# Performance work log

Hardware: AMD Instinct MI355X
Metric: run time of the kernel (lower is better)

Reference implementation:

```python
import jax, jax.numpy as jnp
import numpy as np

S_D, I_D, O_D = 512, 256, 256
BATCH, T = 64, 1024
SNR = 10.0  # noise scale divisor, as in sample_stable_system
SPECTRAL_RADIUS = 0.95  # stable F, mirroring sample_stable_state_matrix


def setup_inputs() -> dict:
    key = jax.random.key(0)
    ks = jax.random.split(key, 9)
    A = np.asarray(jax.random.normal(ks[0], (S_D, S_D), dtype=jnp.float32))
    F = jnp.asarray(A * (SPECTRAL_RADIUS / np.linalg.norm(A, 2)))  # scale to spectral norm 0.95
    B_mat = jax.random.normal(ks[1], (S_D, I_D), dtype=jnp.float32)
    H = jax.random.normal(ks[2], (O_D, S_D), dtype=jnp.float32)
    sqrt_S_W = jax.random.normal(ks[3], (S_D, S_D), dtype=jnp.float32) / SNR
    sqrt_S_V = jax.random.normal(ks[4], (O_D, O_D), dtype=jnp.float32) / SNR
    state = jax.random.normal(ks[5], (BATCH, S_D), dtype=jnp.float32)
    inputs = jax.random.normal(ks[6], (BATCH, T, I_D), dtype=jnp.float32)
    W_noise = jax.random.normal(ks[7], (BATCH, T, S_D), dtype=jnp.float32)
    V_noise = jax.random.normal(ks[8], (BATCH, T, O_D), dtype=jnp.float32)
    return {"state": state, "inputs": inputs, "W_noise": W_noise, "V_noise": V_noise,
            "F": F, "B_mat": B_mat, "H": H, "sqrt_S_W": sqrt_S_W, "sqrt_S_V": sqrt_S_V}


def reference(state, inputs, W_noise, V_noise, F, B_mat, H, sqrt_S_W, sqrt_S_V):
    # Process noise W = eps_W @ sqrt_S_W.T, measurement noise V = eps_V @ sqrt_S_V.T
    W = jnp.einsum('bti,ji->btj', W_noise, sqrt_S_W)          # (B, T, S_D)
    V = jnp.einsum('bti,ji->btj', V_noise, sqrt_S_V)          # (B, T, O_D)
    drive = jnp.einsum('bti,ji->btj', inputs, B_mat) + W      # u_t @ B.T + W_t

    def step(s, u):  # s_t = s_{t-1} @ F.T + u_t
        s = s @ F.T + u
        return s, s

    _, states_t = jax.lax.scan(step, state, jnp.swapaxes(drive, 0, 1))  # (T, B, S_D)
    states = jnp.swapaxes(states_t, 0, 1)                                # (B, T, S_D)
    observations = jnp.einsum('bts,os->bto', states, H) + V              # (B, T, O_D)
    return states, observations
```

## Files before the change

kernel.cpp:

```cpp
#include <hip/hip_runtime.h>
#include <hip/hip_bf16.h>


typedef short bfrag __attribute__((ext_vector_type(8)));
typedef float f32x4 __attribute__((ext_vector_type(4)));

__device__ __host__ inline unsigned short f2bf(float f) {
    union { float f; unsigned u; } x; x.f = f;
    unsigned r = x.u + 0x7fffu + ((x.u >> 16) & 1u);
    return (unsigned short)(r >> 16);
}
__device__ inline float bf2f(unsigned short h) {
    union { unsigned u; float f; } x; x.u = ((unsigned)h) << 16;
    return x.f;
}

#define MSL 262144L

struct GemmDesc {
    const unsigned short* a0; const unsigned short* a1;
    const unsigned short* b;
    float* c;
    const unsigned short* cmbeta;
    unsigned short* cm;
    unsigned short* cmT;
    long a0_base, a0_os, a0_is;
    long a1_base, a1_os, a1_is;
    long a_zq, a_zr;
    long b_base, b_ldb, b_zq, b_zr;
    long c_base, c_os, c_is, c_zq, c_zr;
    long cm_base, cmb_base, cmT_base;
    long a_shift;
    int a0_icl, a1_icl, c_icl, zdivl;
    int ksplit, K, beta;
    int gxl, gyl, gz_main;
    const unsigned short* xa; const unsigned short* xb;
    unsigned short* xcm; unsigned short* xcmT;
};

template<int BM, int BN>
__global__ __launch_bounds__(256) void gemm_k(GemmDesc d) {
    constexpr int MT = BM / 32;
    constexpr int NT = BN / 32;
    __shared__ __align__(16) unsigned short As[2][BM * 64];
    __shared__ __align__(16) unsigned short Bs[2][BN * 64];
    const int tid  = threadIdx.x;
    const int lane = tid & 63;
    const int w    = tid >> 6;
    const int wrow = (w >> 1) * (BM / 2), wcol = (w & 1) * (BN / 2);

    const unsigned nx = gridDim.x, ny = gridDim.y;
    const unsigned nwg = nx * ny * gridDim.z;
    unsigned wid = blockIdx.x + nx * (blockIdx.y + ny * blockIdx.z);
    if ((nwg & 7) == 0) wid = (wid & 7) * (nwg >> 3) + (wid >> 3);
    const int bx = wid & (nx - 1);
    const int by = (wid >> d.gxl) & (ny - 1);
    int bz = wid >> (d.gxl + d.gyl);

    if (bz >= d.gz_main) {
        if (by >= (512 / BM)) return;
        const long za = (long)(bz - d.gz_main) * MSL;
        d.a0 = d.xa; d.a0_base = za; d.a0_os = 512; d.a0_is = 0; d.a0_icl = 0;
        d.a1 = nullptr;
        d.b = d.xb; d.b_base = 0; d.b_ldb = 512; d.b_zq = d.b_zr = 0;
        d.K = 512; d.ksplit = 1 << 30; d.beta = 0; d.a_shift = 0;
        d.a_zq = d.a_zr = 0;
        d.c = nullptr; d.cm = d.xcm; d.cm_base = za;
        d.c_os = 512; d.c_is = 0; d.c_icl = 0; d.c_zq = d.c_zr = 0; d.c_base = 0;
        d.cmT = d.xcmT; d.cmT_base = za;
        bz = 0;
    }
    const long zq = (long)bz >> d.zdivl;
    const long zr = (long)bz & ((1L << d.zdivl) - 1);
    const int row0 = by * BM;
    const int col0 = bx * BN;

    const int g_r = tid >> 3;
    const int g_k = (tid & 7) * 8;
    const int swz = (g_r & 7) << 3;
    const long za_ = zq * d.a_zq + zr * d.a_zr;
    const long zb_ = zq * d.b_zq + zr * d.b_zr;

    const long m0a = (1L << d.a0_icl) - 1, m1a = (1L << d.a1_icl) - 1;
    long a0off[MT], a1off[MT], boff[NT];
#pragma unroll
    for (int i = 0; i < MT; ++i) {
        long ar = (long)row0 + i * 32 + g_r - d.a_shift;
        if (ar < 0) ar = 0;
        a0off[i] = d.a0_base + za_ + (ar >> d.a0_icl) * d.a0_os + (ar & m0a) * d.a0_is;
        a1off[i] = d.a1 ? (d.a1_base + za_ + (ar >> d.a1_icl) * d.a1_os + (ar & m1a) * d.a1_is) : 0;
    }
#pragma unroll
    for (int i = 0; i < NT; ++i)
        boff[i] = d.b_base + zb_ + (long)(col0 + i * 32 + g_r) * d.b_ldb;

    bfrag ar_[MT], br_[NT];
    auto LOADT = [&](int t) {
        const int k0 = t * 64;
        const bool s1 = (k0 >= d.ksplit);
        const int kb = (s1 ? k0 - d.ksplit : k0) + g_k;
        const unsigned short* sp = s1 ? d.a1 : d.a0;
#pragma unroll
        for (int i = 0; i < MT; ++i)
            ar_[i] = *(const bfrag*)(sp + (s1 ? a1off[i] : a0off[i]) + kb);
#pragma unroll
        for (int i = 0; i < NT; ++i) br_[i] = *(const bfrag*)(d.b + boff[i] + k0 + g_k);
    };
    auto WRT = [&](int buf) {
#pragma unroll
        for (int i = 0; i < MT; ++i)
            *(bfrag*)&As[buf][(i * 32 + g_r) * 64 + (g_k ^ swz)] = ar_[i];
#pragma unroll
        for (int i = 0; i < NT; ++i)
            *(bfrag*)&Bs[buf][(i * 32 + g_r) * 64 + (g_k ^ swz)] = br_[i];
    };

    f32x4 acc[MT][NT] = {};
    const int nt = d.K / 64;

    LOADT(0); WRT(0); __syncthreads();
    int cur = 0;
    for (int t = 0; t < nt; ++t) {
        if (t + 1 < nt) LOADT(t + 1);
#pragma unroll
        for (int ks = 0; ks < 2; ++ks) {
            const int kk = ks * 32 + (lane >> 4) * 8;
            bfrag af[MT], bf_[NT];
#pragma unroll
            for (int mt = 0; mt < MT; ++mt) {
                const int r = wrow + mt * 16 + (lane & 15);
                af[mt] = *(const bfrag*)&As[cur][r * 64 + (kk ^ ((r & 7) << 3))];
            }
#pragma unroll
            for (int nn = 0; nn < NT; ++nn) {
                const int r = wcol + nn * 16 + (lane & 15);
                bf_[nn] = *(const bfrag*)&Bs[cur][r * 64 + (kk ^ ((r & 7) << 3))];
            }
#pragma unroll
            for (int mt = 0; mt < MT; ++mt)
#pragma unroll
                for (int nn = 0; nn < NT; ++nn)
                    acc[mt][nn] = __builtin_amdgcn_mfma_f32_16x16x32_bf16(
                        af[mt], bf_[nn], acc[mt][nn], 0, 0, 0);
        }
        if (t + 1 < nt) WRT(cur ^ 1);
        __syncthreads();
        cur ^= 1;
    }

    const long zc = zq * d.c_zq + zr * d.c_zr;
    const long mc = (1L << d.c_icl) - 1;
#pragma unroll
    for (int mt = 0; mt < MT; ++mt) {
        const int rb = row0 + wrow + mt * 16 + ((lane >> 4) << 2);
#pragma unroll
        for (int nn = 0; nn < NT; ++nn) {
            const int cc = col0 + wcol + nn * 16 + (lane & 15);
#pragma unroll
            for (int j = 0; j < 4; ++j) {
                const long r = rb + j;
                const long off = zc + (r >> d.c_icl) * d.c_os + (r & mc) * d.c_is + cc;
                float v = (r < d.a_shift) ? 0.0f : acc[mt][nn][j];
                if (d.beta == 2) v += bf2f(d.cmbeta[d.cmb_base + off]);
                if (d.c)  d.c[d.c_base + off] = v;
                if (d.cm) d.cm[d.cm_base + off] = f2bf(v);
                if (d.cmT) d.cmT[d.cmT_base + zc + (long)cc * 512 + r] = f2bf(v);
            }
        }
    }
}

__global__ __launch_bounds__(512) void p3obs_k(
        const unsigned short* __restrict__ carry, const unsigned short* __restrict__ Gm,
        const unsigned short* __restrict__ Smir, const unsigned short* __restrict__ BopO,
        const float* __restrict__ Vn, float* __restrict__ states, float* __restrict__ obs) {
    __shared__ __align__(16) unsigned char lds[163840];
    unsigned short* As1 = (unsigned short*)(lds);
    unsigned short* Bs1 = (unsigned short*)(lds + 16384);
    unsigned short* Sb  = (unsigned short*)(lds);
    unsigned short* A2  = (unsigned short*)(lds);
    unsigned short* Ts  = (unsigned short*)(lds + 131072);

    const int tid  = threadIdx.x;
    const int lane = tid & 63;
    const int w    = tid >> 6;
    const int wm   = w >> 2, wn = w & 3;
    const int by   = blockIdx.y;
    const int k    = blockIdx.z;
    const unsigned short* G = Gm + (long)k * MSL;

    f32x4 acc[4][8] = {};

    for (int kt = 0; kt < 8; ++kt) {
        __syncthreads();
#pragma unroll
        for (int i = 0; i < 2; ++i) {
            const int fi = tid + i * 512;
            const int row = fi >> 3, kk = (fi & 7) * 8;
            const long rg = (long)by * 128 + row;
            const long c = rg >> 6, b = rg & 63;
            bfrag v = *(const bfrag*)(carry + c * 32768 + b * 512 + kt * 64 + kk);
            *(bfrag*)&As1[row * 64 + (kk ^ ((row & 7) << 3))] = v;
        }
#pragma unroll
        for (int i = 0; i < 8; ++i) {
            const int fi = tid + i * 512;
            const int row = fi >> 3, kk = (fi & 7) * 8;
            bfrag v = *(const bfrag*)(G + (long)row * 512 + kt * 64 + kk);
            *(bfrag*)&Bs1[row * 64 + (kk ^ ((row & 7) << 3))] = v;
        }
        __syncthreads();
#pragma unroll
        for (int ks = 0; ks < 2; ++ks) {
            const int kk = ks * 32 + (lane >> 4) * 8;
            bfrag af[4], bf_[8];
#pragma unroll
            for (int mt = 0; mt < 4; ++mt) {
                const int r = wm * 64 + mt * 16 + (lane & 15);
                af[mt] = *(const bfrag*)&As1[r * 64 + (kk ^ ((r & 7) << 3))];
            }
#pragma unroll
            for (int nt = 0; nt < 8; ++nt) {
                const int n = wn * 128 + nt * 16 + (lane & 15);
                bf_[nt] = *(const bfrag*)&Bs1[n * 64 + (kk ^ ((n & 7) << 3))];
            }
#pragma unroll
            for (int mt = 0; mt < 4; ++mt)
#pragma unroll
                for (int nt = 0; nt < 8; ++nt)
                    acc[mt][nt] = __builtin_amdgcn_mfma_f32_16x16x32_bf16(
                        af[mt], bf_[nt], acc[mt][nt], 0, 0, 0);
        }
    }
    __syncthreads();

#pragma unroll
    for (int mt = 0; mt < 4; ++mt) {
#pragma unroll
        for (int nt = 0; nt < 8; ++nt) {
#pragma unroll
            for (int j = 0; j < 4; ++j) {
                const int lr = wm * 64 + mt * 16 + ((lane >> 4) << 2) + j;
                const int cc = wn * 128 + nt * 16 + (lane & 15);
                const long rg = (long)by * 128 + lr;
                const long c = rg >> 6, b = rg & 63;
                const long t = c * 8 + k;
                float v = acc[mt][nt][j] + bf2f(Smir[b * 524288L + t * 512 + cc]);
                states[b * 524288L + t * 512 + cc] = v;
                Sb[lr * 512 + (cc ^ ((lr & 7) << 3))] = f2bf(v);
            }
        }
    }

    f32x4 acc2[4][4] = {};
    for (int kt = 0; kt < 12; ++kt) {
        __syncthreads();
#pragma unroll
        for (int i = 0; i < 4; ++i) {
            const int fi = tid + i * 512;
            const int row = fi >> 3, kk = (fi & 7) * 8;
            bfrag v = *(const bfrag*)(BopO + (long)row * 768 + kt * 64 + kk);
            *(bfrag*)&Ts[row * 64 + (kk ^ ((row & 7) << 3))] = v;
        }
        if (kt >= 8) {
#pragma unroll
            for (int i = 0; i < 2; ++i) {
                const int fi = tid + i * 512;
                const int row = fi >> 3, kk = (fi & 7) * 8;
                const long rg = (long)by * 128 + row;
                const long c = rg >> 6, b = rg & 63;
                const long t = c * 8 + k;
                const float* p = Vn + b * 262144L + t * 256 + (kt - 8) * 64 + kk;
                f32x4 x0 = *(const f32x4*)p, x1 = *(const f32x4*)(p + 4);
                union { bfrag v; unsigned short h[8]; } u;
#pragma unroll
                for (int q = 0; q < 4; ++q) { u.h[q] = f2bf(x0[q]); u.h[4 + q] = f2bf(x1[q]); }
                *(bfrag*)&A2[row * 64 + (kk ^ ((row & 7) << 3))] = u.v;
            }
        }
        __syncthreads();
#pragma unroll
        for (int ks = 0; ks < 2; ++ks) {
            const int kk = ks * 32 + (lane >> 4) * 8;
            bfrag af[4], bf_[4];
#pragma unroll
            for (int mt = 0; mt < 4; ++mt) {
                const int r = wm * 64 + mt * 16 + (lane & 15);
                af[mt] = (kt < 8)
                    ? *(const bfrag*)&Sb[r * 512 + ((kt * 64 + kk) ^ ((r & 7) << 3))]
                    : *(const bfrag*)&A2[r * 64 + (kk ^ ((r & 7) << 3))];
            }
#pragma unroll
            for (int nt = 0; nt < 4; ++nt) {
                const int n = wn * 64 + nt * 16 + (lane & 15);
                bf_[nt] = *(const bfrag*)&Ts[n * 64 + (kk ^ ((n & 7) << 3))];
            }
#pragma unroll
            for (int mt = 0; mt < 4; ++mt)
#pragma unroll
                for (int nt = 0; nt < 4; ++nt)
                    acc2[mt][nt] = __builtin_amdgcn_mfma_f32_16x16x32_bf16(
                        af[mt], bf_[nt], acc2[mt][nt], 0, 0, 0);
        }
    }
#pragma unroll
    for (int mt = 0; mt < 4; ++mt) {
#pragma unroll
        for (int nt = 0; nt < 4; ++nt) {
#pragma unroll
            for (int j = 0; j < 4; ++j) {
                const int lr = wm * 64 + mt * 16 + ((lane >> 4) << 2) + j;
                const int cc = wn * 64 + nt * 16 + (lane & 15);
                const long rg = (long)by * 128 + lr;
                const long c = rg >> 6, b = rg & 63;
                const long t = c * 8 + k;
                obs[b * 262144L + t * 256 + cc] = acc2[mt][nt][j];
            }
        }
    }
}

__global__ void cvt_k(const float* src, unsigned short* dst, long n) {
    long i = ((long)blockIdx.x * 256 + threadIdx.x) * 8;
    const long stride = (long)gridDim.x * 256 * 8;
    for (; i < n; i += stride) {
        f32x4 x0 = *(const f32x4*)(src + i), x1 = *(const f32x4*)(src + i + 4);
        union { bfrag v; unsigned short h[8]; } t;
#pragma unroll
        for (int q = 0; q < 4; ++q) { t.h[q] = f2bf(x0[q]); t.h[4 + q] = f2bf(x1[q]); }
        *(bfrag*)(dst + i) = t.v;
    }
}

__global__ void build_ops_k(const float* F, const float* Bm, const float* H,
                            const float* sW, const float* sV,
                            unsigned short* bopd, unsigned short* bopo,
                            unsigned short* G1, unsigned short* Gt1) {
    int i = blockIdx.x * 256 + threadIdx.x;
    const int n1 = 512 * 768, n2 = 256 * 768, n3 = 512 * 512;
    if (i < n1) { int n = i / 768, k = i % 768;
        bopd[i] = f2bf(k < 256 ? Bm[n * 256 + k] : sW[n * 512 + (k - 256)]); return; }
    i -= n1;
    if (i < n2) { int o = i / 768, k = i % 768;
        bopo[i] = f2bf(k < 512 ? H[o * 512 + k] : sV[o * 256 + (k - 512)]); return; }
    i -= n2;
    if (i < n3) { G1[i] = f2bf(F[i]); return; }
    i -= n3;
    if (i < n3) { int r = i / 512, c = i % 512; Gt1[i] = f2bf(F[c * 512 + r]); }
}

__global__ void init_carry_k(const float* st0, const unsigned short* Smir,
                             unsigned short* dst) {
    const long i8 = ((long)blockIdx.x * 256 + threadIdx.x) * 8;
    if (i8 >= 4194304L) return;
    const long c = i8 >> 15, rem = i8 & 32767L;
    const long b = rem >> 9, s = rem & 511L;
    union { bfrag v; unsigned short h[8]; } t;
    if (c == 0) {
        const float* p = st0 + b * 512 + s;
        f32x4 x0 = *(const f32x4*)p, x1 = *(const f32x4*)(p + 4);
#pragma unroll
        for (int q = 0; q < 4; ++q) { t.h[q] = f2bf(x0[q]); t.h[4 + q] = f2bf(x1[q]); }
    } else {
        t.v = *(const bfrag*)(Smir + b * 524288L + (c - 1) * 4096L + 3584L + s);
    }
    *(bfrag*)(dst + i8) = t.v;
}

static GemmDesc D0() {
    GemmDesc d = {};
    d.zdivl = 30;
    d.ksplit = 1 << 30;
    d.b_ldb = 512; d.K = 512;
    d.gz_main = 1 << 30;
    return d;
}

extern "C" void kernel_launch(void* const* d_in, const int* in_sizes, int n_in,
                              void* d_out, int out_size, void* d_ws, size_t ws_size,
                              hipStream_t stream) {
    const float* st0 = (const float*)d_in[0];
    const float* inp = (const float*)d_in[1];
    const float* Wn  = (const float*)d_in[2];
    const float* Vn  = (const float*)d_in[3];
    const float* F   = (const float*)d_in[4];
    const float* Bm  = (const float*)d_in[5];
    const float* H   = (const float*)d_in[6];
    const float* sW  = (const float*)d_in[7];
    const float* sV  = (const float*)d_in[8];

    float* states = (float*)d_out;
    float* obs    = states + 33554432L;

    const long MS = MSL;
    const long CB = 32768;
    const int  NC = 128;
    const int  CL = 8;
    const long TOS = 524288;
    const long COS = (long)CL * 512;

    unsigned short* inpb = (unsigned short*)states;
    unsigned short* Wnb  = inpb + 16777216L;

    unsigned short* Smir = (unsigned short*)d_ws;
    unsigned short* G    = Smir + 33554432L;
    unsigned short* Gt   = G + 8 * MS;
    unsigned short* Qb   = Gt + 8 * MS;
    unsigned short* Qtb  = Qb + 6 * MS;
    unsigned short* BopD = Qtb + 6 * MS;
    unsigned short* BopO = BopD + 512 * 768;
    unsigned short* a0m  = BopO + 256 * 768;
    unsigned short* a1m  = a0m + (long)NC * CB;
    (void)in_sizes; (void)n_in; (void)out_size; (void)ws_size;

    auto L128 = [&](const GemmDesc& d, int gx, int gxl, int gy, int gyl, int gz) {
        GemmDesc dd = d; dd.gxl = gxl; dd.gyl = gyl;
        gemm_k<128, 128><<<dim3(gx, gy, gz), dim3(256), 0, stream>>>(dd);
    };
    auto L64 = [&](const GemmDesc& d, int gx, int gxl, int gy, int gyl, int gz) {
        GemmDesc dd = d; dd.gxl = gxl; dd.gyl = gyl;
        gemm_k<64, 64><<<dim3(gx, gy, gz), dim3(256), 0, stream>>>(dd);
    };

    cvt_k<<<dim3(2048), dim3(256), 0, stream>>>(inp, inpb, 16777216L);
    cvt_k<<<dim3(2048), dim3(256), 0, stream>>>(Wn, Wnb, 33554432L);

    build_ops_k<<<dim3(4352), dim3(256), 0, stream>>>(F, Bm, H, sW, sV, BopD, BopO, G, Gt);

    {
        GemmDesc d = D0();
        d.a0 = inpb; d.a0_os = 256;
        d.a1 = Wnb;  d.a1_os = 512;
        d.ksplit = 256; d.K = 768;
        d.b = BopD; d.b_ldb = 768;
        d.cm = Smir; d.c_os = 512;
        L128(d, 4, 2, 512, 9, 1);
    }

    for (int k = 1; k < CL; ++k) {
        GemmDesc d = D0();
        d.a0 = Smir; d.a0_base = (long)(k - 1) * 512;
        d.a0_icl = 7; d.a0_is = COS; d.a0_os = TOS;
        d.b = G;
        d.c_base = (long)k * 512;
        d.c_icl = 7; d.c_is = COS; d.c_os = TOS;
        d.beta = 2; d.cmbeta = Smir; d.cmb_base = (long)k * 512;
        d.cm = Smir; d.cm_base = (long)k * 512;
        d.gz_main = 1;
        int n;
        if (k == 1)      { d.xa = G;           d.xb = Gt;           d.xcm = G + MS;      d.xcmT = Gt + MS;      n = 1; }
        else if (k == 2) { d.xa = G;           d.xb = Gt + MS;      d.xcm = G + 2 * MS;  d.xcmT = Gt + 2 * MS;  n = 2; }
        else if (k == 3) { d.xa = G;           d.xb = Gt + 3 * MS;  d.xcm = G + 4 * MS;  d.xcmT = Gt + 4 * MS;  n = 4; }
        else if (k == 4) { d.xa = G + 7 * MS;  d.xb = Gt + 7 * MS;  d.xcm = Qb;          d.xcmT = Qtb;          n = 1; }
        else             { int j = k - 5;
                           d.xa = Qb + j * MS; d.xb = Qtb + j * MS; d.xcm = Qb + (j+1)*MS; d.xcmT = Qtb + (j+1)*MS; n = 1; }
        L64(d, 8, 3, 128, 7, 1 + n);
    }

    init_carry_k<<<dim3(2048), dim3(256), 0, stream>>>(st0, Smir, a0m);

    unsigned short* curm = a0m;
    unsigned short* nxtm = a1m;
    for (int s = 1; s < NC; s <<= 1) {
        GemmDesc d = D0();
        d.a0 = curm; d.a0_os = 512;
        d.a_shift = (long)s * 64;
        if (s == 1) { d.b = G + 7 * MS; }
        else        { d.b = Qb + (long)(__builtin_ctz(s) - 1) * MS; }
        d.beta = 2; d.cmbeta = curm; d.cmb_base = 0;
        d.cm = nxtm; d.c_os = 512;
        int n = 0;
        if (s == 1) { d.gz_main = 1; d.xa = Qb + 3 * MS; d.xb = Qtb + 3 * MS;
                      d.xcm = Qb + 4 * MS; d.xcmT = Qtb + 4 * MS; n = 1; }
        if (s == 2) { d.gz_main = 1; d.xa = Qb + 4 * MS; d.xb = Qtb + 4 * MS;
                      d.xcm = Qb + 5 * MS; d.xcmT = nullptr; n = 1; }
        L64(d, 8, 3, 128, 7, 1 + n);
        unsigned short* tm = curm; curm = nxtm; nxtm = tm;
    }

    p3obs_k<<<dim3(1, 64, 8), dim3(512), 0, stream>>>(
        curm, G, Smir, BopO, Vn, states, obs);
}
```

Baseline: 621.7 us.

## Use 32x64 GEMM tiles for the scan chain and fold carry init into epilogues

```diff
diff --git a/kernel.cpp b/kernel.cpp
--- a/kernel.cpp
+++ b/kernel.cpp
@@ -24,6 +24,7 @@
     const unsigned short* cmbeta;
     unsigned short* cm;
     unsigned short* cmT;
+    unsigned short* cout;
     long a0_base, a0_os, a0_is;
     long a1_base, a1_os, a1_is;
     long a_zq, a_zr;
@@ -68,6 +69,7 @@
         d.c = nullptr; d.cm = d.xcm; d.cm_base = za;
         d.c_os = 512; d.c_is = 0; d.c_icl = 0; d.c_zq = d.c_zr = 0; d.c_base = 0;
         d.cmT = d.xcmT; d.cmT_base = za;
+        d.cout = nullptr;
         bz = 0;
     }
     const long zq = (long)bz >> d.zdivl;
@@ -115,7 +117,8 @@
             *(bfrag*)&Bs[buf][(i * 32 + g_r) * 64 + (g_k ^ swz)] = br_[i];
     };
 
-    f32x4 acc[MT][NT] = {};
+    constexpr int FR = (BM / 2) / 16;
+    f32x4 acc[FR][NT] = {};
     const int nt = d.K / 64;
 
     LOADT(0); WRT(0); __syncthreads();
@@ -125,9 +128,9 @@
 #pragma unroll
         for (int ks = 0; ks < 2; ++ks) {
             const int kk = ks * 32 + (lane >> 4) * 8;
-            bfrag af[MT], bf_[NT];
-#pragma unroll
-            for (int mt = 0; mt < MT; ++mt) {
+            bfrag af[FR], bf_[NT];
+#pragma unroll
+            for (int mt = 0; mt < FR; ++mt) {
                 const int r = wrow + mt * 16 + (lane & 15);
                 af[mt] = *(const bfrag*)&As[cur][r * 64 + (kk ^ ((r & 7) << 3))];
             }
@@ -137,7 +140,7 @@
                 bf_[nn] = *(const bfrag*)&Bs[cur][r * 64 + (kk ^ ((r & 7) << 3))];
             }
 #pragma unroll
-            for (int mt = 0; mt < MT; ++mt)
+            for (int mt = 0; mt < FR; ++mt)
 #pragma unroll
                 for (int nn = 0; nn < NT; ++nn)
                     acc[mt][nn] = __builtin_amdgcn_mfma_f32_16x16x32_bf16(
@@ -151,7 +154,7 @@
     const long zc = zq * d.c_zq + zr * d.c_zr;
     const long mc = (1L << d.c_icl) - 1;
 #pragma unroll
-    for (int mt = 0; mt < MT; ++mt) {
+    for (int mt = 0; mt < FR; ++mt) {
         const int rb = row0 + wrow + mt * 16 + ((lane >> 4) << 2);
 #pragma unroll
         for (int nn = 0; nn < NT; ++nn) {
@@ -165,6 +168,11 @@
                 if (d.c)  d.c[d.c_base + off] = v;
                 if (d.cm) d.cm[d.cm_base + off] = f2bf(v);
                 if (d.cmT) d.cmT[d.cmT_base + zc + (long)cc * 512 + r] = f2bf(v);
+                if (d.cout) {
+                    const long cr = r & mc, bb = r >> d.c_icl;
+                    if (cr != mc)
+                        d.cout[(cr + 1) * 32768 + bb * 512 + cc] = f2bf(v);
+                }
             }
         }
     }
@@ -333,9 +341,10 @@
 }
 
 __global__ void build_ops_k(const float* F, const float* Bm, const float* H,
-                            const float* sW, const float* sV,
+                            const float* sW, const float* sV, const float* st0,
                             unsigned short* bopd, unsigned short* bopo,
-                            unsigned short* G1, unsigned short* Gt1) {
+                            unsigned short* G1, unsigned short* Gt1,
+                            unsigned short* carry0) {
     int i = blockIdx.x * 256 + threadIdx.x;
     const int n1 = 512 * 768, n2 = 256 * 768, n3 = 512 * 512;
     if (i < n1) { int n = i / 768, k = i % 768;
@@ -346,25 +355,9 @@
     i -= n2;
     if (i < n3) { G1[i] = f2bf(F[i]); return; }
     i -= n3;
-    if (i < n3) { int r = i / 512, c = i % 512; Gt1[i] = f2bf(F[c * 512 + r]); }
-}
-
-__global__ void init_carry_k(const float* st0, const unsigned short* Smir,
-                             unsigned short* dst) {
-    const long i8 = ((long)blockIdx.x * 256 + threadIdx.x) * 8;
-    if (i8 >= 4194304L) return;
-    const long c = i8 >> 15, rem = i8 & 32767L;
-    const long b = rem >> 9, s = rem & 511L;
-    union { bfrag v; unsigned short h[8]; } t;
-    if (c == 0) {
-        const float* p = st0 + b * 512 + s;
-        f32x4 x0 = *(const f32x4*)p, x1 = *(const f32x4*)(p + 4);
-#pragma unroll
-        for (int q = 0; q < 4; ++q) { t.h[q] = f2bf(x0[q]); t.h[4 + q] = f2bf(x1[q]); }
-    } else {
-        t.v = *(const bfrag*)(Smir + b * 524288L + (c - 1) * 4096L + 3584L + s);
-    }
-    *(bfrag*)(dst + i8) = t.v;
+    if (i < n3) { int r = i / 512, c = i % 512; Gt1[i] = f2bf(F[c * 512 + r]); return; }
+    i -= n3;
+    if (i < 32768) carry0[i] = f2bf(st0[i]);
 }
 
 static GemmDesc D0() {
@@ -417,15 +410,16 @@
         GemmDesc dd = d; dd.gxl = gxl; dd.gyl = gyl;
         gemm_k<128, 128><<<dim3(gx, gy, gz), dim3(256), 0, stream>>>(dd);
     };
-    auto L64 = [&](const GemmDesc& d, int gx, int gxl, int gy, int gyl, int gz) {
+    auto L32 = [&](const GemmDesc& d, int gx, int gxl, int gy, int gyl, int gz) {
         GemmDesc dd = d; dd.gxl = gxl; dd.gyl = gyl;
-        gemm_k<64, 64><<<dim3(gx, gy, gz), dim3(256), 0, stream>>>(dd);
+        gemm_k<32, 64><<<dim3(gx, gy, gz), dim3(256), 0, stream>>>(dd);
     };
 
     cvt_k<<<dim3(2048), dim3(256), 0, stream>>>(inp, inpb, 16777216L);
     cvt_k<<<dim3(2048), dim3(256), 0, stream>>>(Wn, Wnb, 33554432L);
 
-    build_ops_k<<<dim3(4352), dim3(256), 0, stream>>>(F, Bm, H, sW, sV, BopD, BopO, G, Gt);
+    build_ops_k<<<dim3(4480), dim3(256), 0, stream>>>(
+        F, Bm, H, sW, sV, st0, BopD, BopO, G, Gt, a0m);
 
     {
         GemmDesc d = D0();
@@ -446,6 +440,7 @@
         d.c_icl = 7; d.c_is = COS; d.c_os = TOS;
         d.beta = 2; d.cmbeta = Smir; d.cmb_base = (long)k * 512;
         d.cm = Smir; d.cm_base = (long)k * 512;
+        if (k == CL - 1) d.cout = a0m;
         d.gz_main = 1;
         int n;
         if (k == 1)      { d.xa = G;           d.xb = Gt;           d.xcm = G + MS;      d.xcmT = Gt + MS;      n = 1; }
@@ -454,10 +449,8 @@
         else if (k == 4) { d.xa = G + 7 * MS;  d.xb = Gt + 7 * MS;  d.xcm = Qb;          d.xcmT = Qtb;          n = 1; }
         else             { int j = k - 5;
                            d.xa = Qb + j * MS; d.xb = Qtb + j * MS; d.xcm = Qb + (j+1)*MS; d.xcmT = Qtb + (j+1)*MS; n = 1; }
-        L64(d, 8, 3, 128, 7, 1 + n);
-    }
-
-    init_carry_k<<<dim3(2048), dim3(256), 0, stream>>>(st0, Smir, a0m);
+        L32(d, 8, 3, 256, 8, 1 + n);
+    }
 
     unsigned short* curm = a0m;
     unsigned short* nxtm = a1m;
@@ -474,7 +467,7 @@
                       d.xcm = Qb + 4 * MS; d.xcmT = Qtb + 4 * MS; n = 1; }
         if (s == 2) { d.gz_main = 1; d.xa = Qb + 4 * MS; d.xb = Qtb + 4 * MS;
                       d.xcm = Qb + 5 * MS; d.xcmT = nullptr; n = 1; }
-        L64(d, 8, 3, 128, 7, 1 + n);
+        L32(d, 8, 3, 256, 8, 1 + n);
         unsigned short* tm = curm; curm = nxtm; nxtm = tm;
     }
 
```

After: 658.0 us. 5.8% more time.
